# Kernel tuning notes

Hardware: AMD Instinct MI355X
Metric: run time of the kernel (lower is better)

## Reference

```python
import jax, jax.numpy as jnp
import numpy as np

N_NODES = 20000
N_EDGES = 400000
B = 4            # number of edge_attr tensors in the Python loop (batch of graphs)
NODE_DIM = 256   # == hidden_dim (required: forward feeds raw x into edge_fc)
EDGE_DIM = 16
HIDDEN = 256
OUT_DIM = 128


def setup_inputs() -> dict:
    key = jax.random.key(0)
    ks = jax.random.split(key, 6)
    x = jax.random.normal(ks[0], (N_NODES, NODE_DIM), dtype=jnp.float32)
    edge_index = jax.random.randint(ks[1], (2, N_EDGES), 0, N_NODES, dtype=jnp.int64)
    edge_attrs = jax.random.normal(ks[2], (B, N_EDGES, EDGE_DIM), dtype=jnp.float32)
    fan_in = 2 * HIDDEN + EDGE_DIM  # edge_fc in_features
    W_edge = jax.random.normal(ks[3], (fan_in, HIDDEN), dtype=jnp.float32) / np.sqrt(fan_in).astype(np.float32)
    b_edge = jnp.zeros((HIDDEN,), dtype=jnp.float32)
    W_graph = jax.random.normal(ks[4], (HIDDEN, OUT_DIM), dtype=jnp.float32) / np.sqrt(HIDDEN).astype(np.float32)
    b_graph = jnp.zeros((OUT_DIM,), dtype=jnp.float32)
    return {"x": x, "edge_index": edge_index, "edge_attrs": edge_attrs,
            "W_edge": W_edge, "b_edge": b_edge, "W_graph": W_graph, "b_graph": b_graph}


def reference(x, edge_index, edge_attrs, W_edge, b_edge, W_graph, b_graph):
    # Original: for each edge_attr in edge_attrs:
    #   relu(cat([x[src], x[dst], edge_attr]) @ W_edge + b).mean(0) @ W_graph + b_graph
    # Equivalent: split W_edge by the concat blocks; the (src,dst) contribution is
    # shared across the batch, so compute it once and broadcast.
    D = x.shape[1]
    W_src, W_dst, W_attr = W_edge[:D], W_edge[D:2 * D], W_edge[2 * D:]
    src = x[edge_index[0]]                      # [E, D] gather
    dst = x[edge_index[1]]                      # [E, D] gather
    base = src @ W_src + dst @ W_dst + b_edge   # [E, H]
    h = jax.nn.relu(base[None, :, :] + jnp.einsum('bea,ah->beh', edge_attrs, W_attr))  # [B, E, H]
    graph_feat = h.mean(axis=1)                 # [B, H] mean pool over edges
    return graph_feat @ W_graph + b_graph       # [B, OUT]
```

## Files before the change

### kernel.cpp

```cpp
#include <hip/hip_runtime.h>

#define N_NODES 20000
#define N_EDGES 400000
#define NODE_DIM 256
#define HIDDEN 256
#define OUT_DIM 128
#define PROJ_BLOCKS 628
#define CONV_BLOCKS 256

typedef __attribute__((ext_vector_type(8))) short short8;
typedef __attribute__((ext_vector_type(4))) float f32x4;

__device__ inline unsigned short f2bf(float f) {
  union { float f; unsigned u; } v; v.f = f;
  unsigned r = (v.u + 0x7FFFu + ((v.u >> 16) & 1u)) >> 16;
  return (unsigned short)r;
}

__global__ __launch_bounds__(256) void proj_mfma(
    const float* __restrict__ x, const float* __restrict__ We,
    const float* __restrict__ be, unsigned short* __restrict__ C,
    float* __restrict__ partial, const float* __restrict__ attrs,
    unsigned short* __restrict__ attrs_bf) {
  const int tid = threadIdx.x;
  if (blockIdx.x >= PROJ_BLOCKS) {
    const int nt = CONV_BLOCKS * 256;
    const int total4 = 4 * N_EDGES * 16 / 4;
    for (int i = (blockIdx.x - PROJ_BLOCKS) * 256 + tid; i < total4; i += nt) {
      float4 v = ((const float4*)attrs)[i];
      ushort4 o;
      o.x = f2bf(v.x); o.y = f2bf(v.y); o.z = f2bf(v.z); o.w = f2bf(v.w);
      ((ushort4*)attrs_bf)[i] = o;
    }
    return;
  }
  if (blockIdx.x == 0) {
    for (int i = tid; i < 4 * HIDDEN; i += 256) partial[i] = 0.f;
  }
  const int bm = blockIdx.x >> 2;
  const int bn = blockIdx.x & 3;
  const int row0 = bm * 128;
  const int col0 = bn * 128;
  const int half = col0 >> 8;
  const int ncol0 = col0 & 255;
  const int lane = tid & 63, wave = tid >> 6;
  const int q = lane >> 4, c = lane & 15;
  const int wm = wave >> 1, wn = wave & 1;

  __shared__ unsigned short As[128][40];
  __shared__ unsigned short Bs[128][40];

  f32x4 acc[4][4];
#pragma unroll
  for (int i = 0; i < 4; ++i)
#pragma unroll
    for (int t = 0; t < 4; ++t) acc[i][t] = (f32x4){0.f, 0.f, 0.f, 0.f};

  const int ar = tid >> 1;
  const int ak = (tid & 1) * 16;
  const int bk = tid >> 3;
  const int bn0 = (tid & 7) * 16;

  for (int k0 = 0; k0 < NODE_DIM; k0 += 32) {
    {
      const int r = row0 + ar;
      short8 t0, t1;
      if (r < N_NODES) {
        const float4* src = (const float4*)&x[(size_t)r * NODE_DIM + k0 + ak];
        float4 f0 = src[0], f1 = src[1], f2 = src[2], f3 = src[3];
        t0[0]=f2bf(f0.x); t0[1]=f2bf(f0.y); t0[2]=f2bf(f0.z); t0[3]=f2bf(f0.w);
        t0[4]=f2bf(f1.x); t0[5]=f2bf(f1.y); t0[6]=f2bf(f1.z); t0[7]=f2bf(f1.w);
        t1[0]=f2bf(f2.x); t1[1]=f2bf(f2.y); t1[2]=f2bf(f2.z); t1[3]=f2bf(f2.w);
        t1[4]=f2bf(f3.x); t1[5]=f2bf(f3.y); t1[6]=f2bf(f3.z); t1[7]=f2bf(f3.w);
      } else {
#pragma unroll
        for (int j = 0; j < 8; ++j) { t0[j] = 0; t1[j] = 0; }
      }
      *(short8*)&As[ar][ak] = t0;
      *(short8*)&As[ar][ak + 8] = t1;
    }
    {
      const float4* src = (const float4*)&We[(size_t)(half * 256 + k0 + bk) * HIDDEN + ncol0 + bn0];
#pragma unroll
      for (int v = 0; v < 4; ++v) {
        float4 f = src[v];
        Bs[bn0 + v * 4 + 0][bk] = f2bf(f.x);
        Bs[bn0 + v * 4 + 1][bk] = f2bf(f.y);
        Bs[bn0 + v * 4 + 2][bk] = f2bf(f.z);
        Bs[bn0 + v * 4 + 3][bk] = f2bf(f.w);
      }
    }
    __syncthreads();
    short8 Af[4], Bf[4];
#pragma unroll
    for (int i = 0; i < 4; ++i) Af[i] = *(const short8*)&As[wm * 64 + i * 16 + c][q * 8];
#pragma unroll
    for (int t = 0; t < 4; ++t) Bf[t] = *(const short8*)&Bs[wn * 64 + t * 16 + c][q * 8];
#pragma unroll
    for (int i = 0; i < 4; ++i)
#pragma unroll
      for (int t = 0; t < 4; ++t)
        acc[i][t] = __builtin_amdgcn_mfma_f32_16x16x32_bf16(Af[i], Bf[t], acc[i][t], 0, 0, 0);
    __syncthreads();
  }

  float biasv[4] = {0.f, 0.f, 0.f, 0.f};
  const int nbase = ncol0 + wn * 64;
  if (half) {
#pragma unroll
    for (int t = 0; t < 4; ++t) biasv[t] = be[nbase + t * 16 + c];
  }
#pragma unroll
  for (int i = 0; i < 4; ++i) {
#pragma unroll
    for (int r = 0; r < 4; ++r) {
      const int node = row0 + wm * 64 + i * 16 + q * 4 + r;
      if (node < N_NODES) {
        ushort4 o;
        o.x = f2bf(acc[i][0][r] + biasv[0]);
        o.y = f2bf(acc[i][1][r] + biasv[1]);
        o.z = f2bf(acc[i][2][r] + biasv[2]);
        o.w = f2bf(acc[i][3][r] + biasv[3]);
        *(ushort4*)&C[(size_t)node * 512 + half * 256 + nbase + c * 4] = o;
      }
    }
  }
}

template <bool PRE>
__global__ __launch_bounds__(256) void edge_mfma(
    const unsigned short* __restrict__ C, const int* __restrict__ ei,
    const float* __restrict__ attrs_f, const unsigned short* __restrict__ attrs_b,
    const float* __restrict__ We, float* __restrict__ partial) {
  const int tid = threadIdx.x;
  const int lane = tid & 63, wave = tid >> 6;
  const int q = lane >> 4, c = lane & 15;
  const int hb = wave * 64;

  short8 Bf[4];
#pragma unroll
  for (int t = 0; t < 4; ++t) {
    short8 bf;
#pragma unroll
    for (int j = 0; j < 8; ++j) {
      int k = q * 8 + j;
      float w = (k < 16) ? We[(size_t)(512 + k) * HIDDEN + hb + t * 16 + c] : 0.0f;
      bf[j] = (short)f2bf(w);
    }
    Bf[t] = bf;
  }

  f32x4 acc4[4][4];
#pragma unroll
  for (int b = 0; b < 4; ++b)
#pragma unroll
    for (int t = 0; t < 4; ++t) acc4[b][t] = (f32x4){0.f, 0.f, 0.f, 0.f};

  const int ngroups = N_EDGES / 16;
  for (int g = blockIdx.x; g < ngroups; g += gridDim.x) {
    const int e0 = g * 16;
    const int4 ns4 = *(const int4*)&ei[e0 + q * 4];
    const int4 nd4 = *(const int4*)&ei[N_EDGES + e0 + q * 4];

    short8 Af[4];
    if (PRE) {
      if (q < 2) {
#pragma unroll
        for (int b = 0; b < 4; ++b)
          Af[b] = *(const short8*)&attrs_b[((size_t)b * N_EDGES + e0 + c) * 16 + q * 8];
      } else {
        short8 z;
#pragma unroll
        for (int j = 0; j < 8; ++j) z[j] = 0;
#pragma unroll
        for (int b = 0; b < 4; ++b) Af[b] = z;
      }
    } else {
      if (q < 2) {
#pragma unroll
        for (int b = 0; b < 4; ++b) {
          const size_t off = ((size_t)b * N_EDGES + e0 + c) * 16 + q * 8;
          const float4 a0 = *(const float4*)&attrs_f[off];
          const float4 a1 = *(const float4*)&attrs_f[off + 4];
          short8 af;
          af[0]=f2bf(a0.x); af[1]=f2bf(a0.y); af[2]=f2bf(a0.z); af[3]=f2bf(a0.w);
          af[4]=f2bf(a1.x); af[5]=f2bf(a1.y); af[6]=f2bf(a1.z); af[7]=f2bf(a1.w);
          Af[b] = af;
        }
      } else {
        short8 z;
#pragma unroll
        for (int j = 0; j < 8; ++j) z[j] = 0;
#pragma unroll
        for (int b = 0; b < 4; ++b) Af[b] = z;
      }
    }

    f32x4 base4[4];
    {
      const int nn[4] = {ns4.x, ns4.y, ns4.z, ns4.w};
      const int dd[4] = {nd4.x, nd4.y, nd4.z, nd4.w};
#pragma unroll
      for (int r = 0; r < 4; ++r) {
        const uint2 s = *(const uint2*)&C[(size_t)nn[r] * 512 + hb + c * 4];
        const uint2 d = *(const uint2*)&C[(size_t)dd[r] * 512 + 256 + hb + c * 4];
        base4[0][r] = __uint_as_float(s.x << 16) + __uint_as_float(d.x << 16);
        base4[1][r] = __uint_as_float(s.x & 0xFFFF0000u) + __uint_as_float(d.x & 0xFFFF0000u);
        base4[2][r] = __uint_as_float(s.y << 16) + __uint_as_float(d.y << 16);
        base4[3][r] = __uint_as_float(s.y & 0xFFFF0000u) + __uint_as_float(d.y & 0xFFFF0000u);
      }
    }

#pragma unroll
    for (int b = 0; b < 4; ++b) {
#pragma unroll
      for (int t = 0; t < 4; ++t) {
        f32x4 u = __builtin_amdgcn_mfma_f32_16x16x32_bf16(Af[b], Bf[t], base4[t], 0, 0, 0);
        u[0] = fmaxf(u[0], 0.f); u[1] = fmaxf(u[1], 0.f);
        u[2] = fmaxf(u[2], 0.f); u[3] = fmaxf(u[3], 0.f);
        acc4[b][t] += u;
      }
    }
  }

#pragma unroll
  for (int b = 0; b < 4; ++b)
#pragma unroll
    for (int t = 0; t < 4; ++t) {
      float v = acc4[b][t][0] + acc4[b][t][1] + acc4[b][t][2] + acc4[b][t][3];
      v += __shfl_xor(v, 16, 64);
      v += __shfl_xor(v, 32, 64);
      if (q == 0) atomicAdd(&partial[b * HIDDEN + hb + t * 16 + c], v);
    }
}

__global__ __launch_bounds__(256) void graph_out(
    const float* __restrict__ partial, const float* __restrict__ Wg,
    const float* __restrict__ bg, float* __restrict__ out) {
  const int o = blockIdx.x;
  const int hh = threadIdx.x;
  const int lane = hh & 63, wave = hh >> 6;
  const float w = Wg[(size_t)hh * OUT_DIM + o];
  float v[4];
#pragma unroll
  for (int b = 0; b < 4; ++b) v[b] = partial[b * HIDDEN + hh] * w;
#pragma unroll
  for (int off = 32; off >= 1; off >>= 1)
#pragma unroll
    for (int b = 0; b < 4; ++b) v[b] += __shfl_down(v[b], off, 64);
  __shared__ float red[4][4];
  if (lane == 0)
#pragma unroll
    for (int b = 0; b < 4; ++b) red[wave][b] = v[b];
  __syncthreads();
  if (hh < 4) {
    float s = red[0][hh] + red[1][hh] + red[2][hh] + red[3][hh];
    out[hh * OUT_DIM + o] = s * (1.0f / (float)N_EDGES) + bg[o];
  }
}

extern "C" void kernel_launch(void* const* d_in, const int* in_sizes, int n_in,
                              void* d_out, int out_size, void* d_ws, size_t ws_size,
                              hipStream_t stream) {
  const float* x  = (const float*)d_in[0];
  const int*   ei = (const int*)d_in[1];
  const float* ea = (const float*)d_in[2];
  const float* We = (const float*)d_in[3];
  const float* be = (const float*)d_in[4];
  const float* Wg = (const float*)d_in[5];
  const float* bg = (const float*)d_in[6];
  float* out = (float*)d_out;

  const size_t C_bytes = (size_t)N_NODES * 512 * 2;
  const size_t A_bytes = (size_t)4 * N_EDGES * 16 * 2;
  unsigned short* C = (unsigned short*)d_ws;
  const bool pre = ws_size >= C_bytes + A_bytes + 4096;
  unsigned short* attrs_bf = pre ? (unsigned short*)((char*)d_ws + C_bytes) : nullptr;
  float* partial = (float*)((char*)d_ws + (pre ? C_bytes + A_bytes : C_bytes));

  const int grid1 = pre ? PROJ_BLOCKS + CONV_BLOCKS : PROJ_BLOCKS;
  proj_mfma<<<grid1, 256, 0, stream>>>(x, We, be, C, partial, ea, attrs_bf);
  if (pre)
    edge_mfma<true><<<2500, 256, 0, stream>>>(C, ei, nullptr, attrs_bf, We, partial);
  else
    edge_mfma<false><<<2500, 256, 0, stream>>>(C, ei, ea, nullptr, We, partial);
  graph_out<<<128, 256, 0, stream>>>(partial, Wg, bg, out);
}
```

Measured before the change: 292.5 us.

## Drop attr bf16 pre-conversion pass, prefetch edge indices, use packed bf16 converts

Removes the separate pass in proj_mfma that converted edge_attrs to bf16 in workspace. edge_mfma now always reads the fp32 attrs directly and converts them in registers, which avoids one full write and read-back of the converted attrs. It also prefetches the next group's edge indices one iteration ahead, and uses the hardware packed float2-to-bf16 conversion in place of manual rounding. The MFMA now starts from a zero accumulator and base is added afterwards, which costs an extra vector add per tile.

```diff
diff --git a/kernel.cpp b/kernel.cpp
--- a/kernel.cpp
+++ b/kernel.cpp
@@ -1,4 +1,5 @@
 #include <hip/hip_runtime.h>
+#include <hip/hip_bf16.h>
 
 #define N_NODES 20000
 #define N_EDGES 400000
@@ -6,11 +7,16 @@
 #define HIDDEN 256
 #define OUT_DIM 128
 #define PROJ_BLOCKS 628
-#define CONV_BLOCKS 256
 
 typedef __attribute__((ext_vector_type(8))) short short8;
 typedef __attribute__((ext_vector_type(4))) float f32x4;
 
+__device__ inline unsigned f2bf_pk(float a, float b) {
+  __hip_bfloat162 h = __float22bfloat162_rn(float2{a, b});
+  union { __hip_bfloat162 h; unsigned u; } v;
+  v.h = h;
+  return v.u;
+}
 __device__ inline unsigned short f2bf(float f) {
   union { float f; unsigned u; } v; v.f = f;
   unsigned r = (v.u + 0x7FFFu + ((v.u >> 16) & 1u)) >> 16;
@@ -20,20 +26,8 @@
 __global__ __launch_bounds__(256) void proj_mfma(
     const float* __restrict__ x, const float* __restrict__ We,
     const float* __restrict__ be, unsigned short* __restrict__ C,
-    float* __restrict__ partial, const float* __restrict__ attrs,
-    unsigned short* __restrict__ attrs_bf) {
+    float* __restrict__ partial) {
   const int tid = threadIdx.x;
-  if (blockIdx.x >= PROJ_BLOCKS) {
-    const int nt = CONV_BLOCKS * 256;
-    const int total4 = 4 * N_EDGES * 16 / 4;
-    for (int i = (blockIdx.x - PROJ_BLOCKS) * 256 + tid; i < total4; i += nt) {
-      float4 v = ((const float4*)attrs)[i];
-      ushort4 o;
-      o.x = f2bf(v.x); o.y = f2bf(v.y); o.z = f2bf(v.z); o.w = f2bf(v.w);
-      ((ushort4*)attrs_bf)[i] = o;
-    }
-    return;
-  }
   if (blockIdx.x == 0) {
     for (int i = tid; i < 4 * HIDDEN; i += 256) partial[i] = 0.f;
   }
@@ -64,20 +58,20 @@
   for (int k0 = 0; k0 < NODE_DIM; k0 += 32) {
     {
       const int r = row0 + ar;
-      short8 t0, t1;
+      union { short8 s; unsigned u[4]; } t0, t1;
       if (r < N_NODES) {
         const float4* src = (const float4*)&x[(size_t)r * NODE_DIM + k0 + ak];
         float4 f0 = src[0], f1 = src[1], f2 = src[2], f3 = src[3];
-        t0[0]=f2bf(f0.x); t0[1]=f2bf(f0.y); t0[2]=f2bf(f0.z); t0[3]=f2bf(f0.w);
-        t0[4]=f2bf(f1.x); t0[5]=f2bf(f1.y); t0[6]=f2bf(f1.z); t0[7]=f2bf(f1.w);
-        t1[0]=f2bf(f2.x); t1[1]=f2bf(f2.y); t1[2]=f2bf(f2.z); t1[3]=f2bf(f2.w);
-        t1[4]=f2bf(f3.x); t1[5]=f2bf(f3.y); t1[6]=f2bf(f3.z); t1[7]=f2bf(f3.w);
+        t0.u[0] = f2bf_pk(f0.x, f0.y); t0.u[1] = f2bf_pk(f0.z, f0.w);
+        t0.u[2] = f2bf_pk(f1.x, f1.y); t0.u[3] = f2bf_pk(f1.z, f1.w);
+        t1.u[0] = f2bf_pk(f2.x, f2.y); t1.u[1] = f2bf_pk(f2.z, f2.w);
+        t1.u[2] = f2bf_pk(f3.x, f3.y); t1.u[3] = f2bf_pk(f3.z, f3.w);
       } else {
-#pragma unroll
-        for (int j = 0; j < 8; ++j) { t0[j] = 0; t1[j] = 0; }
-      }
-      *(short8*)&As[ar][ak] = t0;
-      *(short8*)&As[ar][ak + 8] = t1;
+        t0.u[0] = t0.u[1] = t0.u[2] = t0.u[3] = 0u;
+        t1.u[0] = t1.u[1] = t1.u[2] = t1.u[3] = 0u;
+      }
+      *(short8*)&As[ar][ak] = t0.s;
+      *(short8*)&As[ar][ak + 8] = t1.s;
     }
     {
       const float4* src = (const float4*)&We[(size_t)(half * 256 + k0 + bk) * HIDDEN + ncol0 + bn0];
@@ -116,22 +110,19 @@
     for (int r = 0; r < 4; ++r) {
       const int node = row0 + wm * 64 + i * 16 + q * 4 + r;
       if (node < N_NODES) {
-        ushort4 o;
-        o.x = f2bf(acc[i][0][r] + biasv[0]);
-        o.y = f2bf(acc[i][1][r] + biasv[1]);
-        o.z = f2bf(acc[i][2][r] + biasv[2]);
-        o.w = f2bf(acc[i][3][r] + biasv[3]);
-        *(ushort4*)&C[(size_t)node * 512 + half * 256 + nbase + c * 4] = o;
-      }
-    }
-  }
-}
-
-template <bool PRE>
+        union { ushort4 o; unsigned u[2]; } w;
+        w.u[0] = f2bf_pk(acc[i][0][r] + biasv[0], acc[i][1][r] + biasv[1]);
+        w.u[1] = f2bf_pk(acc[i][2][r] + biasv[2], acc[i][3][r] + biasv[3]);
+        *(ushort4*)&C[(size_t)node * 512 + half * 256 + nbase + c * 4] = w.o;
+      }
+    }
+  }
+}
+
 __global__ __launch_bounds__(256) void edge_mfma(
     const unsigned short* __restrict__ C, const int* __restrict__ ei,
-    const float* __restrict__ attrs_f, const unsigned short* __restrict__ attrs_b,
-    const float* __restrict__ We, float* __restrict__ partial) {
+    const float* __restrict__ attrs, const float* __restrict__ We,
+    float* __restrict__ partial) {
   const int tid = threadIdx.x;
   const int lane = tid & 63, wave = tid >> 6;
   const int q = lane >> 4, c = lane & 15;
@@ -156,44 +147,21 @@
 #pragma unroll
     for (int t = 0; t < 4; ++t) acc4[b][t] = (f32x4){0.f, 0.f, 0.f, 0.f};
 
+  const f32x4 zero4 = {0.f, 0.f, 0.f, 0.f};
   const int ngroups = N_EDGES / 16;
-  for (int g = blockIdx.x; g < ngroups; g += gridDim.x) {
+  int g = blockIdx.x;
+  int4 ns4 = make_int4(0, 0, 0, 0), nd4 = ns4;
+  if (g < ngroups) {
+    ns4 = *(const int4*)&ei[g * 16 + q * 4];
+    nd4 = *(const int4*)&ei[N_EDGES + g * 16 + q * 4];
+  }
+  while (g < ngroups) {
     const int e0 = g * 16;
-    const int4 ns4 = *(const int4*)&ei[e0 + q * 4];
-    const int4 nd4 = *(const int4*)&ei[N_EDGES + e0 + q * 4];
-
-    short8 Af[4];
-    if (PRE) {
-      if (q < 2) {
-#pragma unroll
-        for (int b = 0; b < 4; ++b)
-          Af[b] = *(const short8*)&attrs_b[((size_t)b * N_EDGES + e0 + c) * 16 + q * 8];
-      } else {
-        short8 z;
-#pragma unroll
-        for (int j = 0; j < 8; ++j) z[j] = 0;
-#pragma unroll
-        for (int b = 0; b < 4; ++b) Af[b] = z;
-      }
-    } else {
-      if (q < 2) {
-#pragma unroll
-        for (int b = 0; b < 4; ++b) {
-          const size_t off = ((size_t)b * N_EDGES + e0 + c) * 16 + q * 8;
-          const float4 a0 = *(const float4*)&attrs_f[off];
-          const float4 a1 = *(const float4*)&attrs_f[off + 4];
-          short8 af;
-          af[0]=f2bf(a0.x); af[1]=f2bf(a0.y); af[2]=f2bf(a0.z); af[3]=f2bf(a0.w);
-          af[4]=f2bf(a1.x); af[5]=f2bf(a1.y); af[6]=f2bf(a1.z); af[7]=f2bf(a1.w);
-          Af[b] = af;
-        }
-      } else {
-        short8 z;
-#pragma unroll
-        for (int j = 0; j < 8; ++j) z[j] = 0;
-#pragma unroll
-        for (int b = 0; b < 4; ++b) Af[b] = z;
-      }
+    const int gn = g + gridDim.x;
+    int4 ns4n = ns4, nd4n = nd4;
+    if (gn < ngroups) {
+      ns4n = *(const int4*)&ei[gn * 16 + q * 4];
+      nd4n = *(const int4*)&ei[N_EDGES + gn * 16 + q * 4];
     }
 
     f32x4 base4[4];
@@ -211,16 +179,38 @@
       }
     }
 
+    short8 Af[4];
+    if (q < 2) {
+#pragma unroll
+      for (int b = 0; b < 4; ++b) {
+        const size_t off = ((size_t)b * N_EDGES + e0 + c) * 16 + q * 8;
+        const float4 a0 = *(const float4*)&attrs[off];
+        const float4 a1 = *(const float4*)&attrs[off + 4];
+        union { short8 s; unsigned u[4]; } af;
+        af.u[0] = f2bf_pk(a0.x, a0.y); af.u[1] = f2bf_pk(a0.z, a0.w);
+        af.u[2] = f2bf_pk(a1.x, a1.y); af.u[3] = f2bf_pk(a1.z, a1.w);
+        Af[b] = af.s;
+      }
+    } else {
+      short8 z;
+#pragma unroll
+      for (int j = 0; j < 8; ++j) z[j] = 0;
+#pragma unroll
+      for (int b = 0; b < 4; ++b) Af[b] = z;
+    }
+
 #pragma unroll
     for (int b = 0; b < 4; ++b) {
 #pragma unroll
       for (int t = 0; t < 4; ++t) {
-        f32x4 u = __builtin_amdgcn_mfma_f32_16x16x32_bf16(Af[b], Bf[t], base4[t], 0, 0, 0);
+        f32x4 S = __builtin_amdgcn_mfma_f32_16x16x32_bf16(Af[b], Bf[t], zero4, 0, 0, 0);
+        f32x4 u = S + base4[t];
         u[0] = fmaxf(u[0], 0.f); u[1] = fmaxf(u[1], 0.f);
         u[2] = fmaxf(u[2], 0.f); u[3] = fmaxf(u[3], 0.f);
         acc4[b][t] += u;
       }
     }
+    ns4 = ns4n; nd4 = nd4n; g = gn;
   }
 
 #pragma unroll
@@ -271,18 +261,10 @@
   const float* bg = (const float*)d_in[6];
   float* out = (float*)d_out;
 
-  const size_t C_bytes = (size_t)N_NODES * 512 * 2;
-  const size_t A_bytes = (size_t)4 * N_EDGES * 16 * 2;
   unsigned short* C = (unsigned short*)d_ws;
-  const bool pre = ws_size >= C_bytes + A_bytes + 4096;
-  unsigned short* attrs_bf = pre ? (unsigned short*)((char*)d_ws + C_bytes) : nullptr;
-  float* partial = (float*)((char*)d_ws + (pre ? C_bytes + A_bytes : C_bytes));
-
-  const int grid1 = pre ? PROJ_BLOCKS + CONV_BLOCKS : PROJ_BLOCKS;
-  proj_mfma<<<grid1, 256, 0, stream>>>(x, We, be, C, partial, ea, attrs_bf);
-  if (pre)
-    edge_mfma<true><<<2500, 256, 0, stream>>>(C, ei, nullptr, attrs_bf, We, partial);
-  else
-    edge_mfma<false><<<2500, 256, 0, stream>>>(C, ei, ea, nullptr, We, partial);
+  float* partial = (float*)((char*)d_ws + (size_t)N_NODES * 512 * 2);
+
+  proj_mfma<<<PROJ_BLOCKS, 256, 0, stream>>>(x, We, be, C, partial);
+  edge_mfma<<<2500, 256, 0, stream>>>(C, ei, ea, We, partial);
   graph_out<<<128, 256, 0, stream>>>(partial, Wg, bg, out);
 }
```

New measurement: 291.3 us. About the same (-0.4%).
